# Performance work log

Hardware: AMD Instinct MI355X
Metric: run time of the kernel (lower is better)

## Reference

```python
import jax, jax.numpy as jnp
import numpy as np

B, S, H, N, D = 2, 2048, 1024, 16, 64  # batch, seq, hidden, heads, head_size
PAD = -30000.0


def setup_inputs() -> dict:
    key = jax.random.key(0)
    kx, kqkv, kout, krpe = jax.random.split(key, 4)
    x = jax.random.normal(kx, (B, S, H), jnp.float32)
    qkv = jax.random.normal(kqkv, (H, 3, N, D), jnp.float32) * H ** (-0.5)
    out_w = jax.random.normal(kout, (N, D, H), jnp.float32) * (N * D) ** (-0.5)
    # rpe_bias is zero-init in torch; use small randn so the bias path is exercised
    rpe_bias = jax.random.normal(krpe, (N, S), jnp.float32) * 0.02
    return {"x": x, "qkv": qkv, "out_w": out_w, "rpe_bias": rpe_bias}


def reference(x, qkv, out_w, rpe_bias):
    # q, k, v: [B, N, S, D]
    q, k, v = jnp.einsum('bsx,xMnd->Mbnsd', x, qkv)
    s = x.shape[1]
    a = jnp.einsum('bnsd,bntd->bnst', q, k) * q.shape[-1] ** (-0.5)
    # cumulative relative-position bias: bias[n, i, j] = cumsum(rpe)[n, i-j] for i>=j,
    # PAD otherwise (exactly what to_tril produces on the row-broadcast cumsum).
    cum = jnp.cumsum(rpe_bias[:, :s], axis=-1)            # [N, S]
    rel = jnp.arange(s)[:, None] - jnp.arange(s)[None, :]  # [S, S], i - j
    bias = jnp.where(rel >= 0, cum[:, jnp.clip(rel, 0)], PAD)  # [N, S, S]
    a = jax.nn.softmax(a + bias, axis=-1)
    mix = jnp.einsum('bnst,bntd->bnsd', a, v)
    return jnp.einsum('bnsd,ndx->bsx', mix, out_w)
```

## Files before the change

kernel.cpp:

```cpp
#include <hip/hip_runtime.h>
#include <hip/hip_bf16.h>
#include <cstdint>
#include <cstddef>

#define B_   2
#define S_   2048
#define H_   1024
#define NH   16
#define DH   64
#define LOG2E 1.4426950408889634f
#define SCALE2 (0.125f * LOG2E)

typedef __hip_bfloat16 bf16;
typedef short bf16x8 __attribute__((ext_vector_type(8)));
typedef float f32x4 __attribute__((ext_vector_type(4)));

#define MFMA16(a, b, c) __builtin_amdgcn_mfma_f32_16x16x32_bf16((a), (b), (c), 0, 0, 0)

__device__ __forceinline__ void async16(const void* g, void* l) {
  __builtin_amdgcn_global_load_lds(
      (const __attribute__((address_space(1))) void*)g,
      (__attribute__((address_space(3))) void*)l,
      16, 0, 0);
}

__device__ __forceinline__ void tr_body(const float* __restrict__ src,
                                        bf16* __restrict__ dst, int R, int C,
                                        int c0, int r0, bf16 (*tile)[33], int tid) {
  int tx = tid & 31, ty = tid >> 5;
  for (int i = 0; i < 32; i += 8)
    tile[ty + i][tx] = __float2bfloat16(src[(size_t)(r0 + ty + i) * C + c0 + tx]);
  __syncthreads();
  for (int i = 0; i < 32; i += 8)
    dst[(size_t)(c0 + ty + i) * R + r0 + tx] = tile[tx][ty + i];
}

__global__ __launch_bounds__(256)
void prep(const float* __restrict__ x, bf16* __restrict__ xb,
          const float* __restrict__ qkv, bf16* __restrict__ qkvT,
          const float* __restrict__ outw, bf16* __restrict__ outwT,
          const float* __restrict__ rpe, float* __restrict__ cum) {
  __shared__ char pm[2176] __attribute__((aligned(16)));
  const int L = blockIdx.x, tid = threadIdx.x;
  if (L < 4096) {
    int i = (L * 256 + tid) * 4;
    float4 v = *(const float4*)(x + i);
    bf16 o[4] = {__float2bfloat16(v.x), __float2bfloat16(v.y),
                 __float2bfloat16(v.z), __float2bfloat16(v.w)};
    *(uint64_t*)(xb + i) = *(const uint64_t*)o;
  } else if (L < 7168) {
    int t = L - 4096;
    int cx = t % 96, ry = t / 96;
    tr_body(qkv, qkvT, 1024, 3072, cx * 32, ry * 32, (bf16(*)[33])pm, tid);
  } else if (L < 8192) {
    int t = L - 7168;
    int cx = t & 31, ry = t >> 5;
    tr_body(outw, outwT, 1024, 1024, cx * 32, ry * 32, (bf16(*)[33])pm, tid);
  } else {
    float* ssum = (float*)pm;
    int n = L - 8192;
    float loc[8];
    float s = 0.f;
    int base = tid * 8;
#pragma unroll
    for (int u = 0; u < 8; ++u) {
      loc[u] = rpe[n * S_ + base + u];
      s += loc[u];
    }
    ssum[tid] = s;
    __syncthreads();
    float own = s;
    for (int off = 1; off < 256; off <<= 1) {
      float v = (tid >= off) ? ssum[tid - off] : 0.f;
      __syncthreads();
      ssum[tid] += v;
      __syncthreads();
    }
    float run = ssum[tid] - own;
#pragma unroll
    for (int u = 0; u < 8; ++u) {
      run += loc[u];
      cum[n * S_ + base + u] = run * LOG2E;
    }
  }
}

template <int MODE>
__global__ __launch_bounds__(256, 2)
void gemm_bt(const bf16* __restrict__ A, const bf16* __restrict__ Bt,
             bf16* __restrict__ C0, bf16* __restrict__ C1, bf16* __restrict__ C2,
             float* __restrict__ F0) {
  __shared__ char smem[MODE == 0 ? 36864 : 16384] __attribute__((aligned(16)));
  bf16* As = (bf16*)smem;
  bf16* Bs = (bf16*)(smem + 8192);
  const int tid = threadIdx.x, lane = tid & 63, w = tid >> 6;
  const int lr = lane & 15, lq = lane >> 4;
  const int m0 = blockIdx.y * 128, n0 = blockIdx.x * 128;
  const int wm = (w & 1) * 64, wn = (w >> 1) * 64;

  f32x4 acc[4][4] = {};

  for (int k0 = 0; k0 < 1024; k0 += 32) {
    __syncthreads();
    for (int t = 0; t < 2; ++t) {
      int c = (t * 4 + w) * 64 + lane;
      int row = c >> 2, ch = c & 3;
      int k8 = (ch ^ ((row >> 1) & 3)) * 8;
      async16(A + (size_t)(m0 + row) * 1024 + k0 + k8,
              (char*)As + (size_t)(t * 4 + w) * 1024 + lane * 16);
      async16(Bt + (size_t)(n0 + row) * 1024 + k0 + k8,
              (char*)Bs + (size_t)(t * 4 + w) * 1024 + lane * 16);
    }
    __syncthreads();
    bf16x8 af[4], bfr[4];
#pragma unroll
    for (int mt = 0; mt < 4; ++mt) {
      int row = wm + mt * 16 + lr;
      af[mt] = *(const bf16x8*)(As + row * 32 + ((lq ^ ((row >> 1) & 3)) << 3));
    }
#pragma unroll
    for (int nt = 0; nt < 4; ++nt) {
      int row = wn + nt * 16 + lr;
      bfr[nt] = *(const bf16x8*)(Bs + row * 32 + ((lq ^ ((row >> 1) & 3)) << 3));
    }
#pragma unroll
    for (int mt = 0; mt < 4; ++mt)
#pragma unroll
      for (int nt = 0; nt < 4; ++nt)
        acc[mt][nt] = MFMA16(af[mt], bfr[nt], acc[mt][nt]);
  }

  if (MODE == 0) {
    __syncthreads();
    bf16* E = (bf16*)smem + w * (64 * 72);
    const int cbase = n0 + wn;
    const int mm = cbase >> 10, nn = (cbase >> 6) & 15;
    const int bb = (m0 + wm) >> 11;
    const int sbase = (m0 + wm) & 2047;
    if (mm < 2) {
#pragma unroll
      for (int mt = 0; mt < 4; ++mt)
#pragma unroll
        for (int nt = 0; nt < 4; ++nt)
#pragma unroll
          for (int r = 0; r < 4; ++r)
            E[(mt * 16 + lq * 4 + r) * 72 + nt * 16 + lr] =
                __float2bfloat16(acc[mt][nt][r]);
      bf16* dst = (mm == 0 ? C0 : C1) +
                  ((size_t)(bb * NH + nn) * S_ + sbase) * DH;
#pragma unroll
      for (int it = 0; it < 8; ++it) {
        int c = it * 64 + lane;
        int rw = c >> 3, c8 = c & 7;
        *(uint4*)(dst + (size_t)rw * DH + c8 * 8) =
            *(const uint4*)(E + rw * 72 + c8 * 8);
      }
    } else {
#pragma unroll
      for (int mt = 0; mt < 4; ++mt)
#pragma unroll
        for (int nt = 0; nt < 4; ++nt)
#pragma unroll
          for (int r = 0; r < 4; ++r)
            E[(nt * 16 + lr) * 72 + mt * 16 + lq * 4 + r] =
                __float2bfloat16(acc[mt][nt][r]);
      bf16* dst = C2 + (size_t)(bb * NH + nn) * DH * S_;
#pragma unroll
      for (int it = 0; it < 8; ++it) {
        int c = it * 64 + lane;
        int dr = c >> 3, c8 = c & 7;
        *(uint4*)(dst + (size_t)dr * S_ + sbase + c8 * 8) =
            *(const uint4*)(E + dr * 72 + c8 * 8);
      }
    }
  } else {
#pragma unroll
    for (int mt = 0; mt < 4; ++mt)
#pragma unroll
      for (int nt = 0; nt < 4; ++nt)
#pragma unroll
        for (int r = 0; r < 4; ++r) {
          int rM = m0 + wm + mt * 16 + lq * 4 + r;
          int cN = n0 + wn + nt * 16 + lr;
          F0[(size_t)rM * 1024 + cN] = acc[mt][nt][r];
        }
  }
}

__global__ __launch_bounds__(256, 3)
void fa_kernel(const bf16* __restrict__ q, const bf16* __restrict__ k,
               const bf16* __restrict__ vt, const float* __restrict__ cum,
               bf16* __restrict__ mix) {
  __shared__ char smem[51200] __attribute__((aligned(16)));
  bf16* Ps = (bf16*)(smem + 32768);
  float* cumbuf = (float*)(smem + 50176);

  const int tid = threadIdx.x, lane = tid & 63, w = tid >> 6;
  const int lr = lane & 15, lq = lane >> 4;

  const int L = blockIdx.x;
  const int xcd = L & 7, slot = L >> 3;
  const int bn = xcd + 8 * (slot >> 5);
  const int ti = 31 - (slot & 31);
  const int n = bn & (NH - 1);
  const int b = bn >> 4;
  const float* cumn = cum + n * S_;

  const int i0 = ti * 64;
  const int nj = (ti >> 1) + 1;

  const bf16* qbase = q + ((size_t)bn * S_ + i0 + w * 16) * DH;
  bf16x8 qf[2];
#pragma unroll
  for (int kt = 0; kt < 2; ++kt)
    qf[kt] = *(const bf16x8*)(qbase + lr * DH + kt * 32 + lq * 8);

  f32x4 oacc[4] = {};
  float m_i = -1e30f, l_i = 0.f;
  const int iloc = w * 16 + lr;

  for (int jt = 0; jt < nj; ++jt) {
    const int j0 = jt * 128;
    const bool diag = (jt == nj - 1);
    __syncthreads();

    const char* ksrc = (const char*)(k + ((size_t)bn * S_ + j0) * DH);
#pragma unroll
    for (int t = 0; t < 4; ++t) {
      int cb = t * 4 + w;
      int row = cb * 8 + (lane >> 3);
      int cs = (lane & 7) ^ (row & 7);
      async16(ksrc + row * 128 + cs * 16, smem + cb * 1024 + lane * 16);
    }
    const char* vsrc = (const char*)(vt + (size_t)bn * DH * S_);
#pragma unroll
    for (int t = 0; t < 4; ++t) {
      int cb = t * 4 + w;
      int row = cb * 4 + (lane >> 4);
      int cs = (lane & 15) ^ (row & 15);
      async16(vsrc + (size_t)row * (S_ * 2) + j0 * 2 + cs * 16,
              smem + 16384 + cb * 1024 + lane * 16);
    }
    {
      int src = i0 - j0 - 127 + tid;
      src = src < 0 ? 0 : (src > S_ - 1 ? S_ - 1 : src);
      cumbuf[tid] = cumn[src];
    }
    __syncthreads();

    f32x4 sa[8] = {};
#pragma unroll
    for (int kt = 0; kt < 2; ++kt)
#pragma unroll
      for (int nt = 0; nt < 8; ++nt) {
        int krow = nt * 16 + lr;
        bf16x8 kf = *(const bf16x8*)(smem + krow * 128 +
                        (((kt * 4 + lq) ^ (krow & 7)) << 4));
        sa[nt] = MFMA16(kf, qf[kt], sa[nt]);
      }

    const int doff = i0 - j0;
    float rmax = -1e30f;
    if (!diag) {
#pragma unroll
      for (int nt = 0; nt < 8; ++nt)
#pragma unroll
        for (int r = 0; r < 4; ++r) {
          int rel = iloc - nt * 16 - lq * 4 - r;
          float val = sa[nt][r] * SCALE2 + cumbuf[127 + rel];
          sa[nt][r] = val;
          rmax = fmaxf(rmax, val);
        }
    } else {
#pragma unroll
      for (int nt = 0; nt < 8; ++nt)
#pragma unroll
        for (int r = 0; r < 4; ++r) {
          int rel = iloc - nt * 16 - lq * 4 - r;
          float val = (doff + rel >= 0) ? sa[nt][r] * SCALE2 + cumbuf[127 + rel]
                                        : -1e30f;
          sa[nt][r] = val;
          rmax = fmaxf(rmax, val);
        }
    }
    float mx = fmaxf(rmax, __shfl_xor(rmax, 16));
    mx = fmaxf(mx, __shfl_xor(mx, 32));
    float newm = fmaxf(m_i, mx);
    float al = exp2f(m_i - newm);
    m_i = newm;
    float rs = 0.f;
#pragma unroll
    for (int nt = 0; nt < 8; ++nt)
#pragma unroll
      for (int r = 0; r < 4; ++r) {
        float p = exp2f(sa[nt][r] - newm);
        sa[nt][r] = p;
        rs += p;
      }
    rs += __shfl_xor(rs, 16);
    rs += __shfl_xor(rs, 32);
    l_i = l_i * al + rs;
    float alr[4];
#pragma unroll
    for (int r = 0; r < 4; ++r) alr[r] = __shfl(al, lq * 4 + r);
#pragma unroll
    for (int dt = 0; dt < 4; ++dt)
#pragma unroll
      for (int r = 0; r < 4; ++r) oacc[dt][r] *= alr[r];

#pragma unroll
    for (int nt = 0; nt < 8; ++nt) {
      bf16 pk[4];
#pragma unroll
      for (int r = 0; r < 4; ++r) pk[r] = __float2bfloat16(sa[nt][r]);
      *(uint64_t*)(Ps + iloc * 136 + nt * 16 + lq * 4) = *(const uint64_t*)pk;
    }

#pragma unroll
    for (int kt2 = 0; kt2 < 4; ++kt2) {
      bf16x8 pf = *(const bf16x8*)(Ps + (w * 16 + lr) * 136 + kt2 * 32 + lq * 8);
#pragma unroll
      for (int dt = 0; dt < 4; ++dt) {
        int vrow = dt * 16 + lr;
        bf16x8 vf = *(const bf16x8*)(smem + 16384 + vrow * 256 +
                        (((kt2 * 4 + lq) ^ (vrow & 15)) << 4));
        oacc[dt] = MFMA16(pf, vf, oacc[dt]);
      }
    }
  }

  float lr4[4];
#pragma unroll
  for (int r = 0; r < 4; ++r) lr4[r] = __shfl(l_i, lq * 4 + r);
#pragma unroll
  for (int dt = 0; dt < 4; ++dt)
#pragma unroll
    for (int r = 0; r < 4; ++r) {
      int i = i0 + w * 16 + lq * 4 + r;
      int d = dt * 16 + lr;
      mix[((size_t)(b * S_ + i) * NH + n) * DH + d] =
          __float2bfloat16(oacc[dt][r] / lr4[r]);
    }
}

extern "C" void kernel_launch(void* const* d_in, const int* in_sizes, int n_in,
                              void* d_out, int out_size, void* d_ws, size_t ws_size,
                              hipStream_t stream) {
  const float* x     = (const float*)d_in[0];
  const float* qkv   = (const float*)d_in[1];
  const float* out_w = (const float*)d_in[2];
  const float* rpe   = (const float*)d_in[3];
  float* out = (float*)d_out;

  char* ws = (char*)d_ws;
  bf16* qkvT  = (bf16*)(ws + 0);
  bf16* outwT = (bf16*)(ws + 6291456);
  bf16* xb    = (bf16*)(ws + 8388608);
  bf16* qb    = (bf16*)(ws + 16777216);
  bf16* kb    = (bf16*)(ws + 25165824);
  bf16* vtb   = (bf16*)(ws + 33554432);
  bf16* mixb  = (bf16*)(ws + 41943040);
  float* cum  = (float*)(ws + 50331648);

  prep<<<8208, 256, 0, stream>>>(x, xb, qkv, qkvT, out_w, outwT, rpe, cum);
  gemm_bt<0><<<dim3(3072 / 128, 4096 / 128), 256, 0, stream>>>(xb, qkvT, qb, kb, vtb, nullptr);
  fa_kernel<<<1024, 256, 0, stream>>>(qb, kb, vtb, cum, mixb);
  gemm_bt<1><<<dim3(1024 / 128, 4096 / 128), 256, 0, stream>>>(mixb, outwT, nullptr, nullptr, nullptr, out);
}
```

Baseline: 198.1 us.

## Process 128-row query tiles per block, sharing K/V tiles across two row groups

The flash-attention kernel now handles 128 query rows per block instead of 64, with each wave computing two 16-row groups that reuse the same K and V fragments loaded from shared memory. This halves the number of blocks and the per-row K/V staging traffic, and aligns query tiles with the 128-wide key tiles so the diagonal masking is simpler. The block schedule is also changed to pair long and short causal tiles. In exchange, each block uses more registers and shared memory, so occupancy drops from 3 to 2 blocks per CU, and the grid has fewer blocks for load balancing.

```diff
diff --git a/kernel.cpp b/kernel.cpp
--- a/kernel.cpp
+++ b/kernel.cpp
@@ -187,37 +187,41 @@
   }
 }
 
-__global__ __launch_bounds__(256, 3)
+__global__ __launch_bounds__(256, 2)
 void fa_kernel(const bf16* __restrict__ q, const bf16* __restrict__ k,
                const bf16* __restrict__ vt, const float* __restrict__ cum,
                bf16* __restrict__ mix) {
-  __shared__ char smem[51200] __attribute__((aligned(16)));
+  __shared__ char smem[68608] __attribute__((aligned(16)));
   bf16* Ps = (bf16*)(smem + 32768);
-  float* cumbuf = (float*)(smem + 50176);
+  float* cumbuf = (float*)(smem + 67584);
 
   const int tid = threadIdx.x, lane = tid & 63, w = tid >> 6;
   const int lr = lane & 15, lq = lane >> 4;
 
   const int L = blockIdx.x;
   const int xcd = L & 7, slot = L >> 3;
-  const int bn = xcd + 8 * (slot >> 5);
-  const int ti = 31 - (slot & 31);
+  int bn4, T;
+  if (slot < 32) { bn4 = slot & 3; T = 15 - (slot >> 2); }
+  else           { int s = slot - 32; bn4 = s & 3; T = s >> 2; }
+  const int bn = xcd + 8 * bn4;
   const int n = bn & (NH - 1);
   const int b = bn >> 4;
   const float* cumn = cum + n * S_;
 
-  const int i0 = ti * 64;
-  const int nj = (ti >> 1) + 1;
-
-  const bf16* qbase = q + ((size_t)bn * S_ + i0 + w * 16) * DH;
-  bf16x8 qf[2];
-#pragma unroll
-  for (int kt = 0; kt < 2; ++kt)
-    qf[kt] = *(const bf16x8*)(qbase + lr * DH + kt * 32 + lq * 8);
-
-  f32x4 oacc[4] = {};
-  float m_i = -1e30f, l_i = 0.f;
-  const int iloc = w * 16 + lr;
+  const int i0 = T * 128;
+  const int nj = T + 1;
+
+  bf16x8 qf[2][2];
+#pragma unroll
+  for (int g = 0; g < 2; ++g) {
+    const bf16* qbase = q + ((size_t)bn * S_ + i0 + (g * 4 + w) * 16) * DH;
+#pragma unroll
+    for (int kt = 0; kt < 2; ++kt)
+      qf[g][kt] = *(const bf16x8*)(qbase + lr * DH + kt * 32 + lq * 8);
+  }
+
+  f32x4 oacc[2][4] = {};
+  float m_i[2] = {-1e30f, -1e30f}, l_i[2] = {0.f, 0.f};
 
   for (int jt = 0; jt < nj; ++jt) {
     const int j0 = jt * 128;
@@ -248,7 +252,7 @@
     }
     __syncthreads();
 
-    f32x4 sa[8] = {};
+    f32x4 sa[2][8] = {};
 #pragma unroll
     for (int kt = 0; kt < 2; ++kt)
 #pragma unroll
@@ -256,91 +260,109 @@
         int krow = nt * 16 + lr;
         bf16x8 kf = *(const bf16x8*)(smem + krow * 128 +
                         (((kt * 4 + lq) ^ (krow & 7)) << 4));
-        sa[nt] = MFMA16(kf, qf[kt], sa[nt]);
-      }
-
-    const int doff = i0 - j0;
-    float rmax = -1e30f;
+        sa[0][nt] = MFMA16(kf, qf[0][kt], sa[0][nt]);
+        sa[1][nt] = MFMA16(kf, qf[1][kt], sa[1][nt]);
+      }
+
+    float rmax[2] = {-1e30f, -1e30f};
     if (!diag) {
 #pragma unroll
+      for (int g = 0; g < 2; ++g) {
+        const int iloc = (g * 4 + w) * 16 + lr;
+#pragma unroll
+        for (int nt = 0; nt < 8; ++nt)
+#pragma unroll
+          for (int r = 0; r < 4; ++r) {
+            int rel = iloc - nt * 16 - lq * 4 - r;
+            float val = sa[g][nt][r] * SCALE2 + cumbuf[127 + rel];
+            sa[g][nt][r] = val;
+            rmax[g] = fmaxf(rmax[g], val);
+          }
+      }
+    } else {
+#pragma unroll
+      for (int g = 0; g < 2; ++g) {
+        const int iloc = (g * 4 + w) * 16 + lr;
+#pragma unroll
+        for (int nt = 0; nt < 8; ++nt)
+#pragma unroll
+          for (int r = 0; r < 4; ++r) {
+            int rel = iloc - nt * 16 - lq * 4 - r;
+            float val = (rel >= 0) ? sa[g][nt][r] * SCALE2 + cumbuf[127 + rel]
+                                   : -1e30f;
+            sa[g][nt][r] = val;
+            rmax[g] = fmaxf(rmax[g], val);
+          }
+      }
+    }
+
+#pragma unroll
+    for (int g = 0; g < 2; ++g) {
+      float mx = fmaxf(rmax[g], __shfl_xor(rmax[g], 16));
+      mx = fmaxf(mx, __shfl_xor(mx, 32));
+      float newm = fmaxf(m_i[g], mx);
+      float al = exp2f(m_i[g] - newm);
+      m_i[g] = newm;
+      float rs = 0.f;
+#pragma unroll
       for (int nt = 0; nt < 8; ++nt)
 #pragma unroll
         for (int r = 0; r < 4; ++r) {
-          int rel = iloc - nt * 16 - lq * 4 - r;
-          float val = sa[nt][r] * SCALE2 + cumbuf[127 + rel];
-          sa[nt][r] = val;
-          rmax = fmaxf(rmax, val);
+          float p = exp2f(sa[g][nt][r] - newm);
+          sa[g][nt][r] = p;
+          rs += p;
         }
-    } else {
-#pragma unroll
-      for (int nt = 0; nt < 8; ++nt)
-#pragma unroll
-        for (int r = 0; r < 4; ++r) {
-          int rel = iloc - nt * 16 - lq * 4 - r;
-          float val = (doff + rel >= 0) ? sa[nt][r] * SCALE2 + cumbuf[127 + rel]
-                                        : -1e30f;
-          sa[nt][r] = val;
-          rmax = fmaxf(rmax, val);
-        }
-    }
-    float mx = fmaxf(rmax, __shfl_xor(rmax, 16));
-    mx = fmaxf(mx, __shfl_xor(mx, 32));
-    float newm = fmaxf(m_i, mx);
-    float al = exp2f(m_i - newm);
-    m_i = newm;
-    float rs = 0.f;
-#pragma unroll
-    for (int nt = 0; nt < 8; ++nt)
-#pragma unroll
-      for (int r = 0; r < 4; ++r) {
-        float p = exp2f(sa[nt][r] - newm);
-        sa[nt][r] = p;
-        rs += p;
-      }
-    rs += __shfl_xor(rs, 16);
-    rs += __shfl_xor(rs, 32);
-    l_i = l_i * al + rs;
-    float alr[4];
-#pragma unroll
-    for (int r = 0; r < 4; ++r) alr[r] = __shfl(al, lq * 4 + r);
-#pragma unroll
-    for (int dt = 0; dt < 4; ++dt)
-#pragma unroll
-      for (int r = 0; r < 4; ++r) oacc[dt][r] *= alr[r];
-
-#pragma unroll
-    for (int nt = 0; nt < 8; ++nt) {
-      bf16 pk[4];
-#pragma unroll
-      for (int r = 0; r < 4; ++r) pk[r] = __float2bfloat16(sa[nt][r]);
-      *(uint64_t*)(Ps + iloc * 136 + nt * 16 + lq * 4) = *(const uint64_t*)pk;
+      rs += __shfl_xor(rs, 16);
+      rs += __shfl_xor(rs, 32);
+      l_i[g] = l_i[g] * al + rs;
+      float alr[4];
+#pragma unroll
+      for (int r = 0; r < 4; ++r) alr[r] = __shfl(al, lq * 4 + r);
+#pragma unroll
+      for (int dt = 0; dt < 4; ++dt)
+#pragma unroll
+        for (int r = 0; r < 4; ++r) oacc[g][dt][r] *= alr[r];
+
+      const int prow = (g * 4 + w) * 16 + lr;
+#pragma unroll
+      for (int nt = 0; nt < 8; ++nt) {
+        bf16 pk[4];
+#pragma unroll
+        for (int r = 0; r < 4; ++r) pk[r] = __float2bfloat16(sa[g][nt][r]);
+        *(uint64_t*)(Ps + prow * 136 + nt * 16 + lq * 4) = *(const uint64_t*)pk;
+      }
     }
 
 #pragma unroll
     for (int kt2 = 0; kt2 < 4; ++kt2) {
-      bf16x8 pf = *(const bf16x8*)(Ps + (w * 16 + lr) * 136 + kt2 * 32 + lq * 8);
+      bf16x8 pf0 = *(const bf16x8*)(Ps + (w * 16 + lr) * 136 + kt2 * 32 + lq * 8);
+      bf16x8 pf1 = *(const bf16x8*)(Ps + ((4 + w) * 16 + lr) * 136 + kt2 * 32 + lq * 8);
 #pragma unroll
       for (int dt = 0; dt < 4; ++dt) {
         int vrow = dt * 16 + lr;
         bf16x8 vf = *(const bf16x8*)(smem + 16384 + vrow * 256 +
                         (((kt2 * 4 + lq) ^ (vrow & 15)) << 4));
-        oacc[dt] = MFMA16(pf, vf, oacc[dt]);
-      }
-    }
-  }
-
-  float lr4[4];
-#pragma unroll
-  for (int r = 0; r < 4; ++r) lr4[r] = __shfl(l_i, lq * 4 + r);
-#pragma unroll
-  for (int dt = 0; dt < 4; ++dt)
-#pragma unroll
-    for (int r = 0; r < 4; ++r) {
-      int i = i0 + w * 16 + lq * 4 + r;
-      int d = dt * 16 + lr;
-      mix[((size_t)(b * S_ + i) * NH + n) * DH + d] =
-          __float2bfloat16(oacc[dt][r] / lr4[r]);
-    }
+        oacc[0][dt] = MFMA16(pf0, vf, oacc[0][dt]);
+        oacc[1][dt] = MFMA16(pf1, vf, oacc[1][dt]);
+      }
+    }
+  }
+
+#pragma unroll
+  for (int g = 0; g < 2; ++g) {
+    float lr4[4];
+#pragma unroll
+    for (int r = 0; r < 4; ++r) lr4[r] = __shfl(l_i[g], lq * 4 + r);
+#pragma unroll
+    for (int dt = 0; dt < 4; ++dt)
+#pragma unroll
+      for (int r = 0; r < 4; ++r) {
+        int i = i0 + (g * 4 + w) * 16 + lq * 4 + r;
+        int d = dt * 16 + lr;
+        mix[((size_t)(b * S_ + i) * NH + n) * DH + d] =
+            __float2bfloat16(oacc[g][dt][r] / lr4[r]);
+      }
+  }
 }
 
 extern "C" void kernel_launch(void* const* d_in, const int* in_sizes, int n_in,
@@ -364,6 +386,6 @@
 
   prep<<<8208, 256, 0, stream>>>(x, xb, qkv, qkvT, out_w, outwT, rpe, cum);
   gemm_bt<0><<<dim3(3072 / 128, 4096 / 128), 256, 0, stream>>>(xb, qkvT, qb, kb, vtb, nullptr);
-  fa_kernel<<<1024, 256, 0, stream>>>(qb, kb, vtb, cum, mixb);
+  fa_kernel<<<512, 256, 0, stream>>>(qb, kb, vtb, cum, mixb);
   gemm_bt<1><<<dim3(1024 / 128, 4096 / 128), 256, 0, stream>>>(mixb, outwT, nullptr, nullptr, nullptr, out);
 }
```

After: 218.7 us. 10.4% more time.
